# Kernel tuning notes

Measured on AMD Instinct MI355X. Metric: run time of the kernel, lower is better.

Reference implementation:

```python
import jax, jax.numpy as jnp
import numpy as np


def setup_inputs() -> dict:
    key = jax.random.key(0)
    k1, k2, k3 = jax.random.split(key, 3)
    b, c, h, w = 8, 3, 64, 64
    p = 2048
    y = jax.random.normal(k1, (b, c, h, w), dtype=jnp.float32)
    t = jax.random.normal(k2, (b, p, c), dtype=jnp.float32)
    weights = jax.random.uniform(k3, (c,), dtype=jnp.float32) + 0.5
    return {"y": y, "t": t, "weights": weights}


def reference(y, t, weights):
    # y: [b,c,h,w], t: [b,p,c], weights: [c]
    b, c, h, w = y.shape
    yq = y.reshape(b, c, h * w)  # [b,c,q]
    w2 = weights.astype(yq.dtype) ** 2  # weights applied pre-square -> w^2 in distance
    # ||w*(y-t)||^2 = sum_c w2*t^2 + sum_c w2*y^2 - 2*sum_c w2*t*y
    wy2 = jnp.einsum('bcq,c->bq', yq * yq, w2)          # [b,q]
    wt2 = jnp.einsum('bpc,c->bp', t * t, w2)            # [b,p]
    cross = jnp.einsum('bpc,bcq->bpq', t * w2, yq)      # [b,p,q]
    mse_bpq = wt2[:, :, None] + wy2[:, None, :] - 2.0 * cross  # [b,p,q]
    mse_bp = mse_bpq.min(axis=-1)  # [b,p]
    mse_bq = mse_bpq.min(axis=-2)  # [b,q]
    return mse_bp.mean() + mse_bq.mean()
```

## Files before the change

### kernel.cpp

```cpp
#include <hip/hip_runtime.h>

#define NB 8
#define NQ 4096
#define NP 2048
#define FINF 3.402823466e38f

__global__ __launch_bounds__(256) void chamfer_main(const float* __restrict__ y,
                                                    const float* __restrict__ t,
                                                    const float* __restrict__ w,
                                                    float* __restrict__ blockSums)
{
    __shared__ float4 ldsPts[4096];
    __shared__ float4 ldsQuad[64];

    const int tid = threadIdx.x;
    const int pg  = tid & 3;
    const int s   = tid >> 2;
    const float w0 = w[0]*w[0], w1 = w[1]*w[1], w2 = w[2]*w[2];
    const int blk = blockIdx.x;

    int nStage;

    if (blk < 256) {
        const int b  = blk >> 5;
        const int pb = blk & 31;
        const float* yb = y + (size_t)b * 3 * NQ;
        for (int i = tid; i < NQ; i += 256) {
            const float y0 = yb[i], y1 = yb[NQ + i], y2 = yb[2*NQ + i];
            ldsPts[i] = make_float4(y0, y1, y2, w0*y0*y0 + w1*y1*y1 + w2*y2*y2);
        }
        if (tid < 64) {
            const int p = pb * 64 + tid;
            const float* tp = t + ((size_t)b * NP + p) * 3;
            const float t0 = tp[0], t1 = tp[1], t2 = tp[2];
            ldsQuad[tid] = make_float4(-2.f*w0*t0, -2.f*w1*t1, -2.f*w2*t2,
                                       w0*t0*t0 + w1*t1*t1 + w2*t2*t2);
        }
        nStage = NQ;
    } else {
        const int idx = blk - 256;
        const int b   = idx >> 6;
        const int qb  = idx & 63;
        const float* tb = t + (size_t)b * NP * 3;
        for (int i = tid; i < NP; i += 256) {
            const float t0 = tb[i*3 + 0], t1 = tb[i*3 + 1], t2 = tb[i*3 + 2];
            ldsPts[i] = make_float4(t0, t1, t2, w0*t0*t0 + w1*t1*t1 + w2*t2*t2);
        }
        if (tid < 64) {
            const int q = qb * 64 + tid;
            const float* yb = y + (size_t)b * 3 * NQ;
            const float y0 = yb[q], y1 = yb[NQ + q], y2 = yb[2*NQ + q];
            ldsQuad[tid] = make_float4(-2.f*w0*y0, -2.f*w1*y1, -2.f*w2*y2,
                                       w0*y0*y0 + w1*y1*y1 + w2*y2*y2);
        }
        nStage = NP;
    }
    __syncthreads();

    float4 qd[16];
    float  mm[16];
    #pragma unroll
    for (int r = 0; r < 16; ++r) { qd[r] = ldsQuad[pg*16 + r]; mm[r] = FINF; }

    const int sliceLen = nStage >> 6;
    const float4* myLds = ldsPts + s * sliceLen;
    #pragma unroll 2
    for (int i = 0; i < sliceLen; ++i) {
        const float4 v = myLds[i];
        #pragma unroll
        for (int r = 0; r < 16; ++r) {
            float acc = fmaf(qd[r].x, v.x, v.w);
            acc = fmaf(qd[r].y, v.y, acc);
            acc = fmaf(qd[r].z, v.z, acc);
            mm[r] = fminf(mm[r], acc);
        }
    }
    __syncthreads();

    float* scr = (float*)ldsPts;
    float* scrB = scr + 4096;
    #pragma unroll
    for (int r = 0; r < 16; ++r) scr[s*64 + pg*16 + r] = mm[r];
    __syncthreads();

    {
        const int j  = tid & 63;
        const int s0 = tid >> 6;
        float v = scr[(s0*16 + 0)*64 + j];
        #pragma unroll
        for (int k = 1; k < 16; ++k) v = fminf(v, scr[(s0*16 + k)*64 + j]);
        scrB[s0*64 + j] = v;
    }
    __syncthreads();

    if (tid < 64) {
        float v = fminf(fminf(scrB[tid], scrB[64 + tid]),
                        fminf(scrB[128 + tid], scrB[192 + tid]));
        v += ldsQuad[tid].w;
        for (int off = 32; off > 0; off >>= 1) v += __shfl_down(v, off);
        if (tid == 0) blockSums[blk] = v;
    }
}

__global__ __launch_bounds__(256) void chamfer_final(const float* __restrict__ blockSums,
                                                     float* __restrict__ out)
{
    const int tid = threadIdx.x;
    double sv = (double)blockSums[tid] * (1.0 / (NB * NP))
              + ((double)blockSums[256 + tid] + (double)blockSums[512 + tid]) * (1.0 / (NB * NQ));

    for (int off = 32; off > 0; off >>= 1) sv += __shfl_down(sv, off);

    __shared__ double redd[4];
    const int wave = tid >> 6;
    const int lane = tid & 63;
    if (lane == 0) redd[wave] = sv;
    __syncthreads();
    if (tid == 0) out[0] = (float)(redd[0] + redd[1] + redd[2] + redd[3]);
}

extern "C" void kernel_launch(void* const* d_in, const int* in_sizes, int n_in,
                              void* d_out, int out_size, void* d_ws, size_t ws_size,
                              hipStream_t stream) {
    const float* y = (const float*)d_in[0];
    const float* t = (const float*)d_in[1];
    const float* w = (const float*)d_in[2];
    float* out = (float*)d_out;

    float* blockSums = (float*)d_ws;

    chamfer_main<<<768, 256, 0, stream>>>(y, t, w, blockSums);
    chamfer_final<<<1, 256, 0, stream>>>(blockSums, out);
}
```

Before: 24.72 us.

## Use packed FP32 FMA with SoA-pair LDS layout and rebalance q-side blocks

Stores the staged points as pairs in two LDS arrays so each thread evaluates two points per packed v_pk_fma_f32 and folds the pair with v_min3_f32, halving the number of VALU instructions in the inner loop. The q-side blocks now each own 128 queries with 32 slices, which cuts the grid from 768 to 512 blocks and makes the work per block uniform. Slices are strided and the reduction scratch is padded to avoid LDS bank conflicts. In exchange it adds inline asm and more registers for the broadcast f2 operands, which could reduce occupancy.

```diff
diff --git a/kernel.cpp b/kernel.cpp
--- a/kernel.cpp
+++ b/kernel.cpp
@@ -5,116 +5,151 @@
 #define NP 2048
 #define FINF 3.402823466e38f
 
+typedef float f2 __attribute__((ext_vector_type(2)));
+typedef float f4 __attribute__((ext_vector_type(4)));
+
+__device__ __forceinline__ f2 pk_fma(f2 a, f2 b, f2 c) {
+    f2 d;
+    asm("v_pk_fma_f32 %0, %1, %2, %3" : "=v"(d) : "v"(a), "v"(b), "v"(c));
+    return d;
+}
+__device__ __forceinline__ float min3f(float a, float b, float c) {
+    float d;
+    asm("v_min3_f32 %0, %1, %2, %3" : "=v"(d) : "v"(a), "v"(b), "v"(c));
+    return d;
+}
+
 __global__ __launch_bounds__(256) void chamfer_main(const float* __restrict__ y,
                                                     const float* __restrict__ t,
                                                     const float* __restrict__ w,
                                                     float* __restrict__ blockSums)
 {
-    __shared__ float4 ldsPts[4096];
-    __shared__ float4 ldsQuad[64];
+    __shared__ f4 ldsA[2048];
+    __shared__ f4 ldsB[2048];
+    __shared__ f4 ldsQuad[128];
+    __shared__ float wsum[2];
 
     const int tid = threadIdx.x;
-    const int pg  = tid & 3;
-    const int s   = tid >> 2;
+    const int blk = blockIdx.x;
     const float w0 = w[0]*w[0], w1 = w[1]*w[1], w2 = w[2]*w[2];
-    const int blk = blockIdx.x;
 
-    int nStage;
+    int nOwn, nSlices, pg, s;
 
     if (blk < 256) {
-        const int b  = blk >> 5;
-        const int pb = blk & 31;
+        nOwn = 64; nSlices = 64; pg = tid & 3; s = tid >> 2;
+        const int b = blk >> 5, pb = blk & 31;
         const float* yb = y + (size_t)b * 3 * NQ;
-        for (int i = tid; i < NQ; i += 256) {
-            const float y0 = yb[i], y1 = yb[NQ + i], y2 = yb[2*NQ + i];
-            ldsPts[i] = make_float4(y0, y1, y2, w0*y0*y0 + w1*y1*y1 + w2*y2*y2);
+        const f2* xs = (const f2*)yb;
+        const f2* ys = (const f2*)(yb + NQ);
+        const f2* zs = (const f2*)(yb + 2*NQ);
+        for (int i = tid; i < 2048; i += 256) {
+            const f2 xp = xs[i], yp = ys[i], zp = zs[i];
+            const float n0 = w0*xp.x*xp.x + w1*yp.x*yp.x + w2*zp.x*zp.x;
+            const float n1 = w0*xp.y*xp.y + w1*yp.y*yp.y + w2*zp.y*zp.y;
+            f4 va = {xp.x, xp.y, yp.x, yp.y};
+            f4 vb = {zp.x, zp.y, n0, n1};
+            ldsA[i] = va; ldsB[i] = vb;
         }
         if (tid < 64) {
-            const int p = pb * 64 + tid;
-            const float* tp = t + ((size_t)b * NP + p) * 3;
+            const float* tp = t + ((size_t)b * NP + pb*64 + tid) * 3;
             const float t0 = tp[0], t1 = tp[1], t2 = tp[2];
-            ldsQuad[tid] = make_float4(-2.f*w0*t0, -2.f*w1*t1, -2.f*w2*t2,
-                                       w0*t0*t0 + w1*t1*t1 + w2*t2*t2);
+            f4 q = {-2.f*w0*t0, -2.f*w1*t1, -2.f*w2*t2,
+                    w0*t0*t0 + w1*t1*t1 + w2*t2*t2};
+            ldsQuad[tid] = q;
         }
-        nStage = NQ;
     } else {
+        nOwn = 128; nSlices = 32; pg = tid & 7; s = tid >> 3;
         const int idx = blk - 256;
-        const int b   = idx >> 6;
-        const int qb  = idx & 63;
+        const int b = idx >> 5, qb = idx & 31;
         const float* tb = t + (size_t)b * NP * 3;
-        for (int i = tid; i < NP; i += 256) {
-            const float t0 = tb[i*3 + 0], t1 = tb[i*3 + 1], t2 = tb[i*3 + 2];
-            ldsPts[i] = make_float4(t0, t1, t2, w0*t0*t0 + w1*t1*t1 + w2*t2*t2);
+        for (int i = tid; i < 1024; i += 256) {
+            const f2* tp2 = (const f2*)(tb + i*6);
+            const f2 u0 = tp2[0], u1 = tp2[1], u2 = tp2[2];
+            const float n0 = w0*u0.x*u0.x + w1*u0.y*u0.y + w2*u1.x*u1.x;
+            const float n1 = w0*u1.y*u1.y + w1*u2.x*u2.x + w2*u2.y*u2.y;
+            f4 va = {u0.x, u1.y, u0.y, u2.x};
+            f4 vb = {u1.x, u2.y, n0, n1};
+            ldsA[i] = va; ldsB[i] = vb;
         }
-        if (tid < 64) {
-            const int q = qb * 64 + tid;
+        if (tid < 128) {
             const float* yb = y + (size_t)b * 3 * NQ;
-            const float y0 = yb[q], y1 = yb[NQ + q], y2 = yb[2*NQ + q];
-            ldsQuad[tid] = make_float4(-2.f*w0*y0, -2.f*w1*y1, -2.f*w2*y2,
-                                       w0*y0*y0 + w1*y1*y1 + w2*y2*y2);
-        }
-        nStage = NP;
-    }
-    __syncthreads();
-
-    float4 qd[16];
-    float  mm[16];
-    #pragma unroll
-    for (int r = 0; r < 16; ++r) { qd[r] = ldsQuad[pg*16 + r]; mm[r] = FINF; }
-
-    const int sliceLen = nStage >> 6;
-    const float4* myLds = ldsPts + s * sliceLen;
-    #pragma unroll 2
-    for (int i = 0; i < sliceLen; ++i) {
-        const float4 v = myLds[i];
-        #pragma unroll
-        for (int r = 0; r < 16; ++r) {
-            float acc = fmaf(qd[r].x, v.x, v.w);
-            acc = fmaf(qd[r].y, v.y, acc);
-            acc = fmaf(qd[r].z, v.z, acc);
-            mm[r] = fminf(mm[r], acc);
+            const int q = qb*128 + tid;
+            const float y0 = yb[q], y1 = yb[NQ+q], y2 = yb[2*NQ+q];
+            f4 qv = {-2.f*w0*y0, -2.f*w1*y1, -2.f*w2*y2,
+                     w0*y0*y0 + w1*y1*y1 + w2*y2*y2};
+            ldsQuad[tid] = qv;
         }
     }
     __syncthreads();
 
-    float* scr = (float*)ldsPts;
-    float* scrB = scr + 4096;
+    const int j0 = pg * 16;
+    f2 qx[16], qy[16], qz[16];
+    float mm[16];
     #pragma unroll
-    for (int r = 0; r < 16; ++r) scr[s*64 + pg*16 + r] = mm[r];
-    __syncthreads();
+    for (int r = 0; r < 16; ++r) {
+        const f4 qv = ldsQuad[j0 + r];
+        f2 bx = {qv.x, qv.x}; qx[r] = bx;
+        f2 by = {qv.y, qv.y}; qy[r] = by;
+        f2 bz = {qv.z, qv.z}; qz[r] = bz;
+        mm[r] = FINF;
+    }
 
-    {
-        const int j  = tid & 63;
-        const int s0 = tid >> 6;
-        float v = scr[(s0*16 + 0)*64 + j];
+    const f4* Ap = ldsA + s;
+    const f4* Bp = ldsB + s;
+    #pragma unroll 4
+    for (int j = 0; j < 32; ++j) {
+        const f4 a  = Ap[j * nSlices];
+        const f4 bb = Bp[j * nSlices];
+        const f2 vx = a.xy,  vy = a.zw;
+        const f2 vz = bb.xy, vn = bb.zw;
         #pragma unroll
-        for (int k = 1; k < 16; ++k) v = fminf(v, scr[(s0*16 + k)*64 + j]);
-        scrB[s0*64 + j] = v;
+        for (int r = 0; r < 16; ++r) {
+            f2 acc = pk_fma(qx[r], vx, vn);
+            acc = pk_fma(qy[r], vy, acc);
+            acc = pk_fma(qz[r], vz, acc);
+            mm[r] = min3f(mm[r], acc.x, acc.y);
+        }
     }
     __syncthreads();
 
-    if (tid < 64) {
-        float v = fminf(fminf(scrB[tid], scrB[64 + tid]),
-                        fminf(scrB[128 + tid], scrB[192 + tid]));
+    float* scr = (float*)ldsA;
+    const int SP1 = nSlices + 1;
+    #pragma unroll
+    for (int r = 0; r < 16; ++r) scr[(j0 + r) * SP1 + s] = mm[r];
+    __syncthreads();
+
+    float* scrB = (float*)ldsB;
+    {
+        const int j  = tid & (nOwn - 1);
+        const int s0 = tid / nOwn;
+        float v = FINF;
+        #pragma unroll
+        for (int k = 0; k < 16; ++k) v = fminf(v, scr[j * SP1 + s0*16 + k]);
+        scrB[s0 * nOwn + j] = v;
+    }
+    __syncthreads();
+
+    if (tid < nOwn) {
+        const int nG = 256 / nOwn;
+        float v = scrB[tid];
+        for (int g = 1; g < nG; ++g) v = fminf(v, scrB[g * nOwn + tid]);
         v += ldsQuad[tid].w;
         for (int off = 32; off > 0; off >>= 1) v += __shfl_down(v, off);
-        if (tid == 0) blockSums[blk] = v;
+        if ((tid & 63) == 0) wsum[tid >> 6] = v;
     }
+    __syncthreads();
+    if (tid == 0) blockSums[blk] = (nOwn == 128) ? (wsum[0] + wsum[1]) : wsum[0];
 }
 
-__global__ __launch_bounds__(256) void chamfer_final(const float* __restrict__ blockSums,
+__global__ __launch_bounds__(256) void chamfer_final(const float* __restrict__ bs,
                                                      float* __restrict__ out)
 {
     const int tid = threadIdx.x;
-    double sv = (double)blockSums[tid] * (1.0 / (NB * NP))
-              + ((double)blockSums[256 + tid] + (double)blockSums[512 + tid]) * (1.0 / (NB * NQ));
-
+    double sv = (double)bs[tid] * (1.0 / (NB * NP))
+              + (double)bs[256 + tid] * (1.0 / (NB * NQ));
     for (int off = 32; off > 0; off >>= 1) sv += __shfl_down(sv, off);
-
     __shared__ double redd[4];
-    const int wave = tid >> 6;
-    const int lane = tid & 63;
-    if (lane == 0) redd[wave] = sv;
+    if ((tid & 63) == 0) redd[tid >> 6] = sv;
     __syncthreads();
     if (tid == 0) out[0] = (float)(redd[0] + redd[1] + redd[2] + redd[3]);
 }
@@ -129,6 +164,6 @@
 
     float* blockSums = (float*)d_ws;
 
-    chamfer_main<<<768, 256, 0, stream>>>(y, t, w, blockSums);
+    chamfer_main<<<512, 256, 0, stream>>>(y, t, w, blockSums);
     chamfer_final<<<1, 256, 0, stream>>>(blockSums, out);
 }
```

Result: faster. 20.45 us (-17.3%).
